# Kernel tuning notes

Hardware: AMD Instinct MI355X
Metric: run time of the kernel (lower is better)

The kernel has to match this reference:

```python
import jax, jax.numpy as jnp
import numpy as np

HEAD_NUM = 8
HEAD_DIM = 32
EPS = 0.0  # torch.linalg.norm division has no eps; keep exact


def setup_inputs() -> dict:
    key = jax.random.key(0)
    k1, k2 = jax.random.split(key)
    batch_s = jax.random.normal(k1, (2048, HEAD_NUM * HEAD_DIM), dtype=jnp.float32)
    batch_ro = jax.random.normal(k2, (8192, HEAD_NUM * HEAD_DIM), dtype=jnp.float32)
    return {"batch_s": batch_s, "batch_ro": batch_ro}


def reference(batch_s, batch_ro):
    N, M = batch_s.shape[0], batch_ro.shape[0]
    s = batch_s.reshape(N, HEAD_NUM, HEAD_DIM)   # [N, H, D]
    ro = batch_ro.reshape(M, HEAD_NUM, HEAD_DIM)  # [M, H, D]
    # L2-normalize each head vector
    s = s / jnp.linalg.norm(s, axis=-1, keepdims=True)
    ro = ro / jnp.linalg.norm(ro, axis=-1, keepdims=True)
    # per-head cosine similarity: [N, M, H]
    dist = jnp.einsum('nhd,mhd->nmh', s, ro)
    # max-pool over heads -> [N, M]
    return jnp.max(dist, axis=-1)
```

## Files before the change

kernel.cpp:

```cpp
#include <hip/hip_runtime.h>

#define S_ROWS 2048
#define RO_ROWS 8192
#define HEADS 8
#define HDIM 32
#define ROWLEN 256
#define NB_S (S_ROWS / 16)
#define NB_RO (RO_ROWS / 16)

typedef __attribute__((ext_vector_type(8))) short bf16x8;
typedef __attribute__((ext_vector_type(4))) float f32x4;
typedef __attribute__((ext_vector_type(4))) short s16x4;

__device__ __forceinline__ short f32_to_bf16_rne(float f) {
    union { float f; unsigned u; } v; v.f = f;
    return (short)((v.u + 0x7fffu + ((v.u >> 16) & 1u)) >> 16);
}

__global__ __launch_bounds__(256) void mhd_normalize(const float* __restrict__ s,
                                                     const float* __restrict__ ro,
                                                     short* __restrict__ sF,
                                                     short* __restrict__ roF) {
    const int idx = blockIdx.x * 256 + threadIdx.x;
    const int S_TOT4 = S_ROWS * ROWLEN / 4;
    const bool isS = idx < S_TOT4;
    const int li = isS ? idx : idx - S_TOT4;
    f32x4 x = isS ? ((const f32x4*)s)[li] : ((const f32x4*)ro)[li];
    float ss = x[0] * x[0] + x[1] * x[1] + x[2] * x[2] + x[3] * x[3];
    ss += __shfl_xor(ss, 1);
    ss += __shfl_xor(ss, 2);
    ss += __shfl_xor(ss, 4);
    const float inv = rsqrtf(ss);
    s16x4 r;
    r[0] = f32_to_bf16_rne(x[0] * inv);
    r[1] = f32_to_bf16_rne(x[1] * inv);
    r[2] = f32_to_bf16_rne(x[2] * inv);
    r[3] = f32_to_bf16_rne(x[3] * inv);

    const int n   = li >> 6;
    const int rem = li & 63;
    const int h   = rem >> 3;
    const int dg  = rem & 7;
    const int NB  = isS ? NB_S : NB_RO;
    short* base   = isS ? sF : roF;
    const size_t off = (((size_t)(h * NB + (n >> 4)) * 16 + (n & 15)) * 32) + dg * 4;
    *(s16x4*)(base + off) = r;
}

__global__ __launch_bounds__(256, 4) void mhd_dist(const short* __restrict__ sF,
                                                   const short* __restrict__ roF,
                                                   float* __restrict__ out) {
    __shared__ float lds[4][16][68];
    const int lane = threadIdx.x & 63;
    const int wave = threadIdx.x >> 6;
    const int wr = wave >> 1;
    const int wc = wave & 1;
    const int tile_r = blockIdx.x >> 6;
    const int tile_c = blockIdx.x & 63;
    const int l15 = lane & 15;
    const int kg = lane >> 4;

    f32x4 runmax[4][4];
#pragma unroll
    for (int i = 0; i < 4; ++i)
#pragma unroll
        for (int j = 0; j < 4; ++j)
            runmax[i][j] = (f32x4){-3.0e38f, -3.0e38f, -3.0e38f, -3.0e38f};

    const int nbA = tile_r * 8 + wr * 4;
    const int nbB = tile_c * 8 + wc * 4;
    const size_t laneOff = (size_t)l15 * 32 + kg * 8;

#pragma unroll 1
    for (int h = 0; h < HEADS; ++h) {
        const short* aBase = sF  + (size_t)(h * NB_S  + nbA) * 512 + laneOff;
        const short* bBase = roF + (size_t)(h * NB_RO + nbB) * 512 + laneOff;
        bf16x8 a[4], b[4];
#pragma unroll
        for (int i = 0; i < 4; ++i) {
            a[i] = *(const bf16x8*)(aBase + (size_t)i * 512);
            b[i] = *(const bf16x8*)(bBase + (size_t)i * 512);
        }
#pragma unroll
        for (int i = 0; i < 4; ++i)
#pragma unroll
            for (int j = 0; j < 4; ++j) {
                f32x4 acc = {0.f, 0.f, 0.f, 0.f};
                acc = __builtin_amdgcn_mfma_f32_16x16x32_bf16(b[j], a[i], acc, 0, 0, 0);
#pragma unroll
                for (int q = 0; q < 4; ++q)
                    runmax[i][j][q] = fmaxf(runmax[i][j][q], acc[q]);
            }
    }

    float* outBase = out + (size_t)(tile_r * 128 + wr * 64) * RO_ROWS
                         + tile_c * 128 + wc * 64;
    const int srow = lane >> 4;
    const int scol = (lane & 15) * 4;
#pragma unroll
    for (int i = 0; i < 4; ++i) {
#pragma unroll
        for (int j = 0; j < 4; ++j)
            *(f32x4*)&lds[wave][l15][kg * 4 + j * 16] = runmax[i][j];
#pragma unroll
        for (int t = 0; t < 4; ++t) {
            const int rowL = t * 4 + srow;
            f32x4 v = *(const f32x4*)&lds[wave][rowL][scol];
            *(f32x4*)(outBase + (size_t)(i * 16 + rowL) * RO_ROWS + scol) = v;
        }
    }
}

extern "C" void kernel_launch(void* const* d_in, const int* in_sizes, int n_in,
                              void* d_out, int out_size, void* d_ws, size_t ws_size,
                              hipStream_t stream) {
    const float* batch_s  = (const float*)d_in[0];
    const float* batch_ro = (const float*)d_in[1];
    float* out = (float*)d_out;

    short* sF  = (short*)d_ws;
    short* roF = sF + (size_t)S_ROWS * ROWLEN;

    const int totalV4 = (S_ROWS + RO_ROWS) * ROWLEN / 4;
    mhd_normalize<<<totalV4 / 256, 256, 0, stream>>>(batch_s, batch_ro, sF, roF);

    mhd_dist<<<(S_ROWS / 128) * (RO_ROWS / 128), 256, 0, stream>>>(sF, roF, out);
}
```

Measured before the change: 97.35 us.

## Restructure dist loop to interleave compute with output stores and swizzle tiles

The distance kernel now preloads all eight heads of B fragments into registers. It loops over A row-blocks with an inner head loop, so each 16-row slice of output is finished and stored while later slices are still being computed. This should overlap the large output write traffic with MFMA work, where before all stores waited until the end. A block-index swizzle changes tile order for cache locality, and the normalize kernel now maps threads so that its writes to the packed layout are contiguous. Holding 32 B fragments in registers raises register pressure, and the occupancy hint of 4 is dropped.

```diff
diff --git a/kernel.cpp b/kernel.cpp
--- a/kernel.cpp
+++ b/kernel.cpp
@@ -21,11 +21,18 @@
                                                      const float* __restrict__ ro,
                                                      short* __restrict__ sF,
                                                      short* __restrict__ roF) {
-    const int idx = blockIdx.x * 256 + threadIdx.x;
-    const int S_TOT4 = S_ROWS * ROWLEN / 4;
-    const bool isS = idx < S_TOT4;
-    const int li = isS ? idx : idx - S_TOT4;
-    f32x4 x = isS ? ((const f32x4*)s)[li] : ((const f32x4*)ro)[li];
+    const int v   = blockIdx.x * 256 + threadIdx.x;
+    const int dg  = v & 7;
+    const int r16 = (v >> 3) & 15;
+    const int u   = v >> 7;
+    const int h   = u & 7;
+    const int nb_all = u >> 3;
+    const bool isS = nb_all < NB_S;
+    const int nb  = isS ? nb_all : nb_all - NB_S;
+    const int n   = nb * 16 + r16;
+
+    const float* src = isS ? s : ro;
+    f32x4 x = *(const f32x4*)(src + (size_t)n * ROWLEN + h * HDIM + dg * 4);
     float ss = x[0] * x[0] + x[1] * x[1] + x[2] * x[2] + x[3] * x[3];
     ss += __shfl_xor(ss, 1);
     ss += __shfl_xor(ss, 2);
@@ -37,76 +44,70 @@
     r[2] = f32_to_bf16_rne(x[2] * inv);
     r[3] = f32_to_bf16_rne(x[3] * inv);
 
-    const int n   = li >> 6;
-    const int rem = li & 63;
-    const int h   = rem >> 3;
-    const int dg  = rem & 7;
-    const int NB  = isS ? NB_S : NB_RO;
-    short* base   = isS ? sF : roF;
-    const size_t off = (((size_t)(h * NB + (n >> 4)) * 16 + (n & 15)) * 32) + dg * 4;
-    *(s16x4*)(base + off) = r;
+    short* dst = isS ? sF : roF;
+    const int NB = isS ? NB_S : NB_RO;
+    *(s16x4*)(dst + ((size_t)(h * NB + nb) * 16 + r16) * 32 + dg * 4) = r;
 }
 
-__global__ __launch_bounds__(256, 4) void mhd_dist(const short* __restrict__ sF,
-                                                   const short* __restrict__ roF,
-                                                   float* __restrict__ out) {
+__global__ __launch_bounds__(256) void mhd_dist(const short* __restrict__ sF,
+                                                const short* __restrict__ roF,
+                                                float* __restrict__ out) {
     __shared__ float lds[4][16][68];
     const int lane = threadIdx.x & 63;
     const int wave = threadIdx.x >> 6;
     const int wr = wave >> 1;
     const int wc = wave & 1;
-    const int tile_r = blockIdx.x >> 6;
-    const int tile_c = blockIdx.x & 63;
+    const int bid = blockIdx.x;
+    const int swz = (bid & 7) * 128 + (bid >> 3);
+    const int tile_r = swz >> 6;
+    const int tile_c = swz & 63;
     const int l15 = lane & 15;
     const int kg = lane >> 4;
-
-    f32x4 runmax[4][4];
-#pragma unroll
-    for (int i = 0; i < 4; ++i)
-#pragma unroll
-        for (int j = 0; j < 4; ++j)
-            runmax[i][j] = (f32x4){-3.0e38f, -3.0e38f, -3.0e38f, -3.0e38f};
 
     const int nbA = tile_r * 8 + wr * 4;
     const int nbB = tile_c * 8 + wc * 4;
     const size_t laneOff = (size_t)l15 * 32 + kg * 8;
 
-#pragma unroll 1
-    for (int h = 0; h < HEADS; ++h) {
-        const short* aBase = sF  + (size_t)(h * NB_S  + nbA) * 512 + laneOff;
-        const short* bBase = roF + (size_t)(h * NB_RO + nbB) * 512 + laneOff;
-        bf16x8 a[4], b[4];
+    bf16x8 B[HEADS][4];
 #pragma unroll
-        for (int i = 0; i < 4; ++i) {
-            a[i] = *(const bf16x8*)(aBase + (size_t)i * 512);
-            b[i] = *(const bf16x8*)(bBase + (size_t)i * 512);
-        }
+    for (int h = 0; h < HEADS; ++h)
 #pragma unroll
-        for (int i = 0; i < 4; ++i)
-#pragma unroll
-            for (int j = 0; j < 4; ++j) {
-                f32x4 acc = {0.f, 0.f, 0.f, 0.f};
-                acc = __builtin_amdgcn_mfma_f32_16x16x32_bf16(b[j], a[i], acc, 0, 0, 0);
-#pragma unroll
-                for (int q = 0; q < 4; ++q)
-                    runmax[i][j][q] = fmaxf(runmax[i][j][q], acc[q]);
-            }
-    }
+        for (int j = 0; j < 4; ++j)
+            B[h][j] = *(const bf16x8*)(roF + (size_t)(h * NB_RO + nbB + j) * 512 + laneOff);
 
     float* outBase = out + (size_t)(tile_r * 128 + wr * 64) * RO_ROWS
                          + tile_c * 128 + wc * 64;
     const int srow = lane >> 4;
     const int scol = (lane & 15) * 4;
+
 #pragma unroll
     for (int i = 0; i < 4; ++i) {
+        f32x4 runmax[4];
 #pragma unroll
         for (int j = 0; j < 4; ++j)
-            *(f32x4*)&lds[wave][l15][kg * 4 + j * 16] = runmax[i][j];
+            runmax[j] = (f32x4){-3.0e38f, -3.0e38f, -3.0e38f, -3.0e38f};
+
+#pragma unroll
+        for (int h = 0; h < HEADS; ++h) {
+            const bf16x8 a = *(const bf16x8*)(sF + (size_t)(h * NB_S + nbA + i) * 512 + laneOff);
+#pragma unroll
+            for (int j = 0; j < 4; ++j) {
+                f32x4 acc = {0.f, 0.f, 0.f, 0.f};
+                acc = __builtin_amdgcn_mfma_f32_16x16x32_bf16(B[h][j], a, acc, 0, 0, 0);
+#pragma unroll
+                for (int q = 0; q < 4; ++q)
+                    runmax[j][q] = fmaxf(runmax[j][q], acc[q]);
+            }
+        }
+
+#pragma unroll
+        for (int j = 0; j < 4; ++j)
+            *(f32x4*)&lds[wave][l15][kg * 4 + j * 16] = runmax[j];
 #pragma unroll
         for (int t = 0; t < 4; ++t) {
             const int rowL = t * 4 + srow;
-            f32x4 v = *(const f32x4*)&lds[wave][rowL][scol];
-            *(f32x4*)(outBase + (size_t)(i * 16 + rowL) * RO_ROWS + scol) = v;
+            f32x4 vv = *(const f32x4*)&lds[wave][rowL][scol];
+            *(f32x4*)(outBase + (size_t)(i * 16 + rowL) * RO_ROWS + scol) = vv;
         }
     }
 }
```

New measurement: 102.6 us. 1.05x slower.
